# Kernel optimization log

Measured on AMD Instinct MI355X. Metric: run time of the kernel, lower is better.

Reference implementation:

```python
import jax, jax.numpy as jnp
import numpy as np
import math

B, L, H, D = 4, 2048, 8, 64
FACTOR = 5
SAMPLE_K = min(FACTOR * math.ceil(math.log(L)), L)   # u = 40
N_TOP = min(FACTOR * math.ceil(math.log(L)), L)      # U_part = 40


def setup_inputs() -> dict:
    key = jax.random.key(0)
    k1, k2, k3, k4 = jax.random.split(key, 4)
    return {
        "queries": jax.random.normal(k1, (B, L, H, D), dtype=jnp.float32),
        "keys": jax.random.normal(k2, (B, L, H, D), dtype=jnp.float32),
        "values": jax.random.normal(k3, (B, L, H, D), dtype=jnp.float32),
        "index_sample": jax.random.randint(k4, (L, SAMPLE_K), 0, L, dtype=jnp.int32),
    }


def reference(queries, keys, values, index_sample):
    # queries/keys/values: [B, L, H, D] -> [B, H, L, D]
    Q = jnp.transpose(queries, (0, 2, 1, 3))
    K = jnp.transpose(keys, (0, 2, 1, 3))
    V = jnp.transpose(values, (0, 2, 1, 3))
    Bc, Hc, L_Q, Dc = Q.shape
    L_K = K.shape[2]
    scale = 1.0 / math.sqrt(Dc)

    # --- _prob_QK: random K sampling, sparsity measure M, top-n_top queries ---
    K_samp = K[:, :, index_sample, :]                       # [B,H,L_Q,S,D]
    QK_samp = jnp.einsum('bhqd,bhqsd->bhqs', Q, K_samp)     # [B,H,L_Q,S]
    M = QK_samp.max(axis=-1) - QK_samp.sum(axis=-1) / L_K   # [B,H,L_Q]
    _, M_top = jax.lax.top_k(M, N_TOP)                      # [B,H,n_top]
    Q_reduce = jnp.take_along_axis(Q, M_top[..., None], axis=2)  # [B,H,n_top,D]
    scores = jnp.einsum('bhud,bhkd->bhuk', Q_reduce, K) * scale  # [B,H,n_top,L_K]

    # --- initial context (mask_flag=False): mean of V broadcast over queries ---
    context = jnp.broadcast_to(V.mean(axis=2, keepdims=True), (Bc, Hc, L_Q, Dc))

    # --- update context at selected query positions ---
    attn = jax.nn.softmax(scores, axis=-1)                  # [B,H,n_top,L_K]
    upd = jnp.einsum('bhuk,bhkd->bhud', attn, V)            # [B,H,n_top,D]
    bi = jnp.arange(Bc)[:, None, None]
    hi = jnp.arange(Hc)[None, :, None]
    context = context.at[bi, hi, M_top].set(upd)

    return jnp.transpose(context, (0, 2, 1, 3))             # [B,L_Q,H,D]
```

## Files before the change

### kernel.cpp

```cpp
#include <hip/hip_runtime.h>
#include <math.h>

#define B_ 4
#define L_ 2048
#define H_ 8
#define D_ 64
#define SK 40
#define NTOP 40
#define HD (H_*D_)

typedef float4 f4;

static __device__ __forceinline__ float rl(float v, int l) {
  return __int_as_float(__builtin_amdgcn_readlane(__float_as_int(v), l));
}

static __device__ __forceinline__ int xcd_swz(int bid, int cpx) {
  return (bid & 7) * cpx + (bid >> 3);
}

__global__ __launch_bounds__(256) void k_sampleM(
    const float* __restrict__ Q, const float* __restrict__ K,
    const int* __restrict__ samp, float* __restrict__ M)
{
  int bid = xcd_swz(blockIdx.x, 256);
  int w = threadIdx.x >> 6, lane = threadIdx.x & 63;
  int g = lane >> 3, li = lane & 7;
  int gq = (bid * 4 + w) * 8 + g;
  int qpos = gq & (L_ - 1);
  int bh = gq >> 11;
  int h = bh & (H_ - 1), b = bh >> 3;
  const size_t bhoff = (size_t)b * L_ * HD + (size_t)h * D_;
  const f4* qrow = (const f4*)(Q + bhoff + (size_t)qpos * HD);
  f4 q0 = qrow[li], q1 = qrow[li + 8];
  const int* srow = samp + qpos * SK;
  const float* kb = K + bhoff;
  float mx = -INFINITY, sm = 0.f;
  #pragma unroll 4
  for (int s = 0; s < SK; ++s) {
    int ki = srow[s];
    const f4* krow = (const f4*)(kb + (size_t)ki * HD);
    f4 k0 = krow[li], k1 = krow[li + 8];
    float p = q0.x*k0.x + q0.y*k0.y + q0.z*k0.z + q0.w*k0.w
            + q1.x*k1.x + q1.y*k1.y + q1.z*k1.z + q1.w*k1.w;
    p += __shfl_xor(p, 1);
    p += __shfl_xor(p, 2);
    p += __shfl_xor(p, 4);
    mx = fmaxf(mx, p);
    sm += p;
  }
  if (li == 0) M[gq] = mx - sm * (1.0f / L_);
}

__global__ __launch_bounds__(256) void k_topk(
    const float* __restrict__ M, int* __restrict__ top)
{
  __shared__ unsigned hist[256];
  __shared__ unsigned sfx[256];
  __shared__ int s_sel, s_k;
  __shared__ unsigned s_ngt, s_neq;
  __shared__ int eqidx[L_];
  int bh = blockIdx.x, t = threadIdx.x;

  unsigned v[8];
  #pragma unroll
  for (int j = 0; j < 8; ++j) {
    unsigned u = __float_as_uint(M[bh * L_ + t + j * 256]);
    v[j] = (u & 0x80000000u) ? ~u : (u | 0x80000000u);
  }

  unsigned prefix = 0;
  int kneed = NTOP;
  for (int shift = 24; shift >= 0; shift -= 8) {
    hist[t] = 0;
    __syncthreads();
    unsigned msk = (shift == 24) ? 0u : (0xFFFFFFFFu << (shift + 8));
    #pragma unroll
    for (int j = 0; j < 8; ++j)
      if ((v[j] & msk) == prefix)
        atomicAdd(&hist[(v[j] >> shift) & 255u], 1u);
    __syncthreads();
    sfx[t] = hist[t];
    __syncthreads();
    #pragma unroll
    for (int off = 1; off < 256; off <<= 1) {
      unsigned add = (t + off < 256) ? sfx[t + off] : 0u;
      __syncthreads();
      sfx[t] += add;
      __syncthreads();
    }
    unsigned Sm = sfx[t];
    unsigned Sn = (t < 255) ? sfx[t + 1] : 0u;
    if (Sm >= (unsigned)kneed && Sn < (unsigned)kneed) {
      s_sel = t;
      s_k = kneed - (int)Sn;
    }
    __syncthreads();
    prefix |= ((unsigned)s_sel) << shift;
    kneed = s_k;
  }
  if (t == 0) { s_ngt = 0; s_neq = 0; }
  __syncthreads();
  #pragma unroll
  for (int j = 0; j < 8; ++j) {
    if (v[j] > prefix) {
      unsigned p = atomicAdd(&s_ngt, 1u);
      top[bh * NTOP + p] = t + j * 256;
    } else if (v[j] == prefix) {
      unsigned p = atomicAdd(&s_neq, 1u);
      eqidx[p] = t + j * 256;
    }
  }
  __syncthreads();
  if (t == 0) {
    int base = NTOP - kneed;
    int n = (int)s_neq;
    for (int r = 0; r < kneed; ++r) {
      int bm = 0x7fffffff, bp = 0;
      for (int i = 0; i < n; ++i)
        if (eqidx[i] < bm) { bm = eqidx[i]; bp = i; }
      top[bh * NTOP + base + r] = bm;
      eqidx[bp] = 0x7fffffff;
    }
  }
}

__global__ __launch_bounds__(256) void k_vmean1(
    const float* __restrict__ V, float* __restrict__ part)
{
  __shared__ f4 red[16][16];
  int bh = blockIdx.x >> 5, chunk = blockIdx.x & 31;
  int h = bh & 7, b = bh >> 3;
  int t = threadIdx.x;
  int d4 = t & 15, rg = t >> 4;
  const f4* vb = (const f4*)(V + (size_t)b * L_ * HD + (size_t)h * D_);
  f4 s = {0.f, 0.f, 0.f, 0.f};
  int row0 = chunk * 64 + rg;
  #pragma unroll
  for (int r = 0; r < 4; ++r) {
    f4 v = vb[(size_t)(row0 + r * 16) * (HD / 4) + d4];
    s.x += v.x; s.y += v.y; s.z += v.z; s.w += v.w;
  }
  red[rg][d4] = s;
  __syncthreads();
  #pragma unroll
  for (int off = 8; off; off >>= 1) {
    if (rg < off) {
      f4 a = red[rg][d4], bb = red[rg + off][d4];
      a.x += bb.x; a.y += bb.y; a.z += bb.z; a.w += bb.w;
      red[rg][d4] = a;
    }
    __syncthreads();
  }
  if (rg == 0) ((f4*)part)[(size_t)blockIdx.x * 16 + d4] = red[0][d4];
}

__global__ __launch_bounds__(64) void k_vmean2(
    const float* __restrict__ part, float* __restrict__ vm)
{
  int bh = blockIdx.x, lane = threadIdx.x;
  float s = 0.f;
  #pragma unroll 8
  for (int c = 0; c < 32; ++c)
    s += part[(size_t)(bh * 32 + c) * 64 + lane];
  vm[bh * 64 + lane] = s * (1.0f / L_);
}

__global__ __launch_bounds__(256) void k_fill(
    const float* __restrict__ vm, float* __restrict__ out)
{
  int i = blockIdx.x * 256 + threadIdx.x;
  int d4 = i & 15;
  int h  = (i >> 4) & 7;
  int b  = i >> 18;
  ((f4*)out)[i] = ((const f4*)vm)[(b * 8 + h) * 16 + d4];
}

__global__ __launch_bounds__(256) void k_attn(
    const float* __restrict__ Q, const float* __restrict__ K,
    const float* __restrict__ V, const int* __restrict__ top,
    float* __restrict__ pm, float* __restrict__ pl, float* __restrict__ pacc)
{
  __shared__ float plds[4][5][64];
  int bid = xcd_swz(blockIdx.x, 256);
  int lane = threadIdx.x & 63;
  int w = __builtin_amdgcn_readfirstlane(threadIdx.x >> 6);
  int gw = bid * 4 + w;
  int uq = gw & 7;
  int ch = (gw >> 3) & 31;
  int bh = gw >> 8;
  int h = bh & 7, b = bh >> 3;
  const size_t bhoff = (size_t)b * L_ * HD + (size_t)h * D_;
  const int kbase = ch * 64;

  f4 kr[16];
  {
    const f4* krow = (const f4*)(K + bhoff + (size_t)(kbase + lane) * HD);
    #pragma unroll
    for (int j = 0; j < 16; ++j) kr[j] = krow[j];
  }
  const float* qr[5];
  #pragma unroll
  for (int u = 0; u < 5; ++u) {
    int pos = __builtin_amdgcn_readfirstlane(top[bh * NTOP + uq * 5 + u]);
    qr[u] = Q + bhoff + (size_t)pos * HD;
  }
  float s[5] = {0.f, 0.f, 0.f, 0.f, 0.f};
  #pragma unroll
  for (int j = 0; j < 16; ++j) {
    f4 kv = kr[j];
    #pragma unroll
    for (int u = 0; u < 5; ++u) {
      s[u] = fmaf(qr[u][4*j+0], kv.x, s[u]);
      s[u] = fmaf(qr[u][4*j+1], kv.y, s[u]);
      s[u] = fmaf(qr[u][4*j+2], kv.z, s[u]);
      s[u] = fmaf(qr[u][4*j+3], kv.w, s[u]);
    }
  }
  #pragma unroll
  for (int u = 0; u < 5; ++u) {
    float sv = s[u] * 0.125f;
    float mx = sv;
    #pragma unroll
    for (int off = 32; off; off >>= 1) mx = fmaxf(mx, __shfl_xor(mx, off));
    float pv = __expf(sv - mx);
    float ls = pv;
    #pragma unroll
    for (int off = 32; off; off >>= 1) ls += __shfl_xor(ls, off);
    plds[w][u][lane] = pv;
    int e = (bh * 32 + ch) * NTOP + uq * 5 + u;
    if (lane == 0) { pm[e] = mx; pl[e] = ls; }
  }
  __syncthreads();
  float acc[5] = {0.f, 0.f, 0.f, 0.f, 0.f};
  const float* vb = V + bhoff + (size_t)kbase * HD + lane;
  const f4* pw = (const f4*)&plds[w][0][0];
  #pragma unroll
  for (int j = 0; j < 16; ++j) {
    float vv0 = vb[(size_t)(4*j+0) * HD];
    float vv1 = vb[(size_t)(4*j+1) * HD];
    float vv2 = vb[(size_t)(4*j+2) * HD];
    float vv3 = vb[(size_t)(4*j+3) * HD];
    f4 pj[5];
    #pragma unroll
    for (int u = 0; u < 5; ++u) pj[u] = pw[u * 16 + j];
    #pragma unroll
    for (int u = 0; u < 5; ++u) {
      acc[u] = fmaf(pj[u].x, vv0, acc[u]);
      acc[u] = fmaf(pj[u].y, vv1, acc[u]);
      acc[u] = fmaf(pj[u].z, vv2, acc[u]);
      acc[u] = fmaf(pj[u].w, vv3, acc[u]);
    }
  }
  #pragma unroll
  for (int u = 0; u < 5; ++u) {
    size_t e = (size_t)(bh * 32 + ch) * NTOP + uq * 5 + u;
    pacc[e * 64 + lane] = acc[u];
  }
}

__global__ __launch_bounds__(256) void k_merge(
    const float* __restrict__ pm, const float* __restrict__ pl,
    const float* __restrict__ pacc, const int* __restrict__ top,
    float* __restrict__ out)
{
  int w = threadIdx.x >> 6, lane = threadIdx.x & 63;
  int gw = blockIdx.x * 4 + w;
  int bh = gw / NTOP, u = gw - bh * NTOP;
  int h = bh & 7, b = bh >> 3;
  int c = lane & 31;
  int e = (bh * 32 + c) * NTOP + u;
  float mc = pm[e], lc = pl[e];
  if (lane >= 32) { mc = -INFINITY; lc = 0.f; }
  float Mg = mc;
  #pragma unroll
  for (int off = 32; off; off >>= 1) Mg = fmaxf(Mg, __shfl_xor(Mg, off));
  float fc = __expf(mc - Mg);
  float fl = fc * lc;
  float Lg = fl;
  #pragma unroll
  for (int off = 32; off; off >>= 1) Lg += __shfl_xor(Lg, off);
  float o = 0.f;
  const float* pa = pacc + ((size_t)(bh * 32) * NTOP + u) * 64 + lane;
  #pragma unroll
  for (int cc = 0; cc < 32; ++cc)
    o = fmaf(rl(fc, cc), pa[(size_t)cc * NTOP * 64], o);
  int pos = top[bh * NTOP + u];
  out[((size_t)(b * L_ + pos) * H_ + h) * D_ + lane] = o / Lg;
}

extern "C" void kernel_launch(void* const* d_in, const int* in_sizes, int n_in,
                              void* d_out, int out_size, void* d_ws, size_t ws_size,
                              hipStream_t stream) {
  const float* Q = (const float*)d_in[0];
  const float* K = (const float*)d_in[1];
  const float* V = (const float*)d_in[2];
  const int* samp = (const int*)d_in[3];
  float* out = (float*)d_out;

  float* ws    = (float*)d_ws;
  float* M     = ws;
  float* vmean = M + 65536;
  float* pm    = vmean + 2048;
  float* pl    = pm + 40960;
  float* pacc  = pl + 40960;
  int*   top   = (int*)(pacc + 2621440);
  float* vpart = pacc;

  hipLaunchKernelGGL(k_sampleM, dim3(2048), dim3(256), 0, stream, Q, K, samp, M);
  hipLaunchKernelGGL(k_topk,   dim3(32),   dim3(256), 0, stream, M, top);
  hipLaunchKernelGGL(k_vmean1, dim3(1024), dim3(256), 0, stream, V, vpart);
  hipLaunchKernelGGL(k_vmean2, dim3(32),   dim3(64),  0, stream, vpart, vmean);
  hipLaunchKernelGGL(k_fill,   dim3(4096), dim3(256), 0, stream, vmean, out);
  hipLaunchKernelGGL(k_attn,   dim3(2048), dim3(256), 0, stream, Q, K, V, top, pm, pl, pacc);
  hipLaunchKernelGGL(k_merge,  dim3(320),  dim3(256), 0, stream, pm, pl, pacc, top, out);
}
```

Before: 84.04 us.

## Stage K/V chunk in LDS once per block and process all 40 queries per block

k_attn now assigns one (b,h,chunk) to each block instead of splitting the 40 top queries across 8 warps in separate blocks. The 64-key K tile (XOR-swizzled) and the V tile are loaded cooperatively into shared memory once. Each warp then handles 10 queries, reading K and V from LDS. This removes the repeated global reads of the same K/V chunk by several blocks and halves the grid. In exchange it uses more registers and LDS per block (about 33KB) and gives fewer blocks, which may lower occupancy.

```diff
diff --git a/kernel.cpp b/kernel.cpp
--- a/kernel.cpp
+++ b/kernel.cpp
@@ -181,44 +181,58 @@
     const float* __restrict__ V, const int* __restrict__ top,
     float* __restrict__ pm, float* __restrict__ pl, float* __restrict__ pacc)
 {
-  __shared__ float plds[4][5][64];
-  int bid = xcd_swz(blockIdx.x, 256);
-  int lane = threadIdx.x & 63;
-  int w = __builtin_amdgcn_readfirstlane(threadIdx.x >> 6);
-  int gw = bid * 4 + w;
-  int uq = gw & 7;
-  int ch = (gw >> 3) & 31;
-  int bh = gw >> 8;
+  __shared__ f4 Kl4[1024];
+  __shared__ float Vlds[4096];
+  __shared__ float plds[4][10][64];
+  int bid = xcd_swz(blockIdx.x, 128);
+  int t = threadIdx.x;
+  int lane = t & 63;
+  int w = __builtin_amdgcn_readfirstlane(t >> 6);
+  int ch = bid & 31;
+  int bh = bid >> 5;
   int h = bh & 7, b = bh >> 3;
   const size_t bhoff = (size_t)b * L_ * HD + (size_t)h * D_;
   const int kbase = ch * 64;
 
-  f4 kr[16];
-  {
-    const f4* krow = (const f4*)(K + bhoff + (size_t)(kbase + lane) * HD);
-    #pragma unroll
-    for (int j = 0; j < 16; ++j) kr[j] = krow[j];
-  }
-  const float* qr[5];
-  #pragma unroll
-  for (int u = 0; u < 5; ++u) {
-    int pos = __builtin_amdgcn_readfirstlane(top[bh * NTOP + uq * 5 + u]);
-    qr[u] = Q + bhoff + (size_t)pos * HD;
-  }
-  float s[5] = {0.f, 0.f, 0.f, 0.f, 0.f};
+  const f4* kgb = (const f4*)(K + bhoff);
+  const f4* vgb = (const f4*)(V + bhoff);
+  f4 ks[4], vs[4];
+  #pragma unroll
+  for (int i = 0; i < 4; ++i) {
+    int n = t + 256 * i;
+    int r = n >> 4, ss = n & 15;
+    ks[i] = kgb[(size_t)(kbase + r) * (HD/4) + (ss ^ (r & 7))];
+    vs[i] = vgb[(size_t)(kbase + r) * (HD/4) + ss];
+  }
+  const float* qr_[10];
+  #pragma unroll
+  for (int u = 0; u < 10; ++u) {
+    int pos = __builtin_amdgcn_readfirstlane(top[bh * NTOP + w * 10 + u]);
+    qr_[u] = Q + bhoff + (size_t)pos * HD;
+  }
+  #pragma unroll
+  for (int i = 0; i < 4; ++i) Kl4[t + 256 * i] = ks[i];
+  #pragma unroll
+  for (int i = 0; i < 4; ++i) ((f4*)Vlds)[t + 256 * i] = vs[i];
+  __syncthreads();
+
+  float s[10];
+  #pragma unroll
+  for (int u = 0; u < 10; ++u) s[u] = 0.f;
+  int sbase = lane * 16, smask = lane & 7;
   #pragma unroll
   for (int j = 0; j < 16; ++j) {
-    f4 kv = kr[j];
-    #pragma unroll
-    for (int u = 0; u < 5; ++u) {
-      s[u] = fmaf(qr[u][4*j+0], kv.x, s[u]);
-      s[u] = fmaf(qr[u][4*j+1], kv.y, s[u]);
-      s[u] = fmaf(qr[u][4*j+2], kv.z, s[u]);
-      s[u] = fmaf(qr[u][4*j+3], kv.w, s[u]);
-    }
-  }
-  #pragma unroll
-  for (int u = 0; u < 5; ++u) {
+    f4 kv = Kl4[sbase + (j ^ smask)];
+    #pragma unroll
+    for (int u = 0; u < 10; ++u) {
+      s[u] = fmaf(qr_[u][4*j+0], kv.x, s[u]);
+      s[u] = fmaf(qr_[u][4*j+1], kv.y, s[u]);
+      s[u] = fmaf(qr_[u][4*j+2], kv.z, s[u]);
+      s[u] = fmaf(qr_[u][4*j+3], kv.w, s[u]);
+    }
+  }
+  #pragma unroll
+  for (int u = 0; u < 10; ++u) {
     float sv = s[u] * 0.125f;
     float mx = sv;
     #pragma unroll
@@ -228,33 +242,31 @@
     #pragma unroll
     for (int off = 32; off; off >>= 1) ls += __shfl_xor(ls, off);
     plds[w][u][lane] = pv;
-    int e = (bh * 32 + ch) * NTOP + uq * 5 + u;
+    int e = (bh * 32 + ch) * NTOP + w * 10 + u;
     if (lane == 0) { pm[e] = mx; pl[e] = ls; }
   }
-  __syncthreads();
-  float acc[5] = {0.f, 0.f, 0.f, 0.f, 0.f};
-  const float* vb = V + bhoff + (size_t)kbase * HD + lane;
+  float acc[10];
+  #pragma unroll
+  for (int u = 0; u < 10; ++u) acc[u] = 0.f;
   const f4* pw = (const f4*)&plds[w][0][0];
   #pragma unroll
   for (int j = 0; j < 16; ++j) {
-    float vv0 = vb[(size_t)(4*j+0) * HD];
-    float vv1 = vb[(size_t)(4*j+1) * HD];
-    float vv2 = vb[(size_t)(4*j+2) * HD];
-    float vv3 = vb[(size_t)(4*j+3) * HD];
-    f4 pj[5];
-    #pragma unroll
-    for (int u = 0; u < 5; ++u) pj[u] = pw[u * 16 + j];
-    #pragma unroll
-    for (int u = 0; u < 5; ++u) {
-      acc[u] = fmaf(pj[u].x, vv0, acc[u]);
-      acc[u] = fmaf(pj[u].y, vv1, acc[u]);
-      acc[u] = fmaf(pj[u].z, vv2, acc[u]);
-      acc[u] = fmaf(pj[u].w, vv3, acc[u]);
-    }
-  }
-  #pragma unroll
-  for (int u = 0; u < 5; ++u) {
-    size_t e = (size_t)(bh * 32 + ch) * NTOP + uq * 5 + u;
+    float vv0 = Vlds[(4*j+0)*64 + lane];
+    float vv1 = Vlds[(4*j+1)*64 + lane];
+    float vv2 = Vlds[(4*j+2)*64 + lane];
+    float vv3 = Vlds[(4*j+3)*64 + lane];
+    #pragma unroll
+    for (int u = 0; u < 10; ++u) {
+      f4 pj = pw[u * 16 + j];
+      acc[u] = fmaf(pj.x, vv0, acc[u]);
+      acc[u] = fmaf(pj.y, vv1, acc[u]);
+      acc[u] = fmaf(pj.z, vv2, acc[u]);
+      acc[u] = fmaf(pj.w, vv3, acc[u]);
+    }
+  }
+  #pragma unroll
+  for (int u = 0; u < 10; ++u) {
+    size_t e = (size_t)(bh * 32 + ch) * NTOP + w * 10 + u;
     pacc[e * 64 + lane] = acc[u];
   }
 }
@@ -312,6 +324,6 @@
   hipLaunchKernelGGL(k_vmean1, dim3(1024), dim3(256), 0, stream, V, vpart);
   hipLaunchKernelGGL(k_vmean2, dim3(32),   dim3(64),  0, stream, vpart, vmean);
   hipLaunchKernelGGL(k_fill,   dim3(4096), dim3(256), 0, stream, vmean, out);
-  hipLaunchKernelGGL(k_attn,   dim3(2048), dim3(256), 0, stream, Q, K, V, top, pm, pl, pacc);
+  hipLaunchKernelGGL(k_attn,   dim3(1024), dim3(256), 0, stream, Q, K, V, top, pm, pl, pacc);
   hipLaunchKernelGGL(k_merge,  dim3(320),  dim3(256), 0, stream, pm, pl, pacc, top, out);
 }
```

New measurement: 98.33 us. 17.0% more time.
